# Kernel optimization log

Measured on AMD Instinct MI355X. Metric: run time of the kernel, lower is better.

The kernel has to match this reference:

```python
import jax, jax.numpy as jnp
import numpy as np

B, C, H = 16, 512, 32
HID, NB, S, P, SR = 512, 36, 26, 7, 2
SCALE = 32.0
N_LOC, N_LOC_LAB = 12, 8
N_GRP, GRP_SZ, N_GRP_LAB = 4, 6, 16
IN_DIM = P * P * C


def roi_align(feat, coords, scale, pooled, sr):
    # feat: (B,C,H,W); coords: (B,NB,4) normalized xyxy. torchvision roi_align,
    # aligned=False, fixed sampling_ratio=sr (adaptive ratio is data-dependent).
    Bs, Cc, Hh, Ww = feat.shape
    x1 = coords[..., 0] * scale
    y1 = coords[..., 1] * scale
    x2 = coords[..., 2] * scale
    y2 = coords[..., 3] * scale
    rw = jnp.maximum(x2 - x1, 1.0)
    rh = jnp.maximum(y2 - y1, 1.0)
    bw = rw / pooled
    bh = rh / pooled
    # sample offsets within roi, in bin units: (pooled*sr,)
    off = (jnp.arange(pooled)[:, None] + (jnp.arange(sr) + 0.5) / sr).reshape(-1)
    ys = y1[..., None] + off * bh[..., None]  # (B,NB,pooled*sr)
    xs = x1[..., None] + off * bw[..., None]

    def prep(t, size):
        valid = (t > -1.0) & (t < size)
        tc = jnp.clip(t, 0.0, size - 1)
        lo = jnp.floor(tc).astype(jnp.int32)
        hi = jnp.minimum(lo + 1, size - 1)
        frac = tc - lo
        return lo, hi, frac, valid

    y_lo, y_hi, ly, vy = prep(ys, Hh)
    x_lo, x_hi, lx, vx = prep(xs, Ww)
    hy, hx = 1.0 - ly, 1.0 - lx

    featl = feat.transpose(0, 2, 3, 1)  # (B,H,W,C)
    b_idx = jnp.arange(Bs)[:, None, None, None]

    def gather(yi, xi):
        # -> (B,NB,Py,Px,C)
        return featl[b_idx, yi[:, :, :, None], xi[:, :, None, :]]

    def w(a, b):
        return (a[..., :, None] * b[..., None, :])[..., None]

    val = (gather(y_lo, x_lo) * w(hy, hx) + gather(y_lo, x_hi) * w(hy, lx)
           + gather(y_hi, x_lo) * w(ly, hx) + gather(y_hi, x_hi) * w(ly, lx))
    mask = (vy[:, :, :, None] & vx[:, :, None, :])[..., None]
    val = jnp.where(mask, val, 0.0)
    val = val.reshape(Bs, -1, pooled, sr, pooled, sr, Cc).mean(axis=(3, 5))
    return val.transpose(0, 1, 4, 2, 3)  # (B,NB,C,pooled,pooled)


def setup_inputs() -> dict:
    key = jax.random.key(0)
    ks = jax.random.split(key, 10)
    lf = jax.random.normal(ks[0], (B, C, H, H), dtype=jnp.float32)
    xs = jnp.sort(jax.random.uniform(ks[1], (B, S, 2)), axis=-1)
    ys = jnp.sort(jax.random.uniform(ks[2], (B, S, 2)), axis=-1)
    coords = jnp.stack([xs[..., 0], ys[..., 0], xs[..., 1], ys[..., 1]], axis=-1)
    sc = 0.02
    return {
        'local_features': lf,
        'pred_bbox_coords': coords,
        'roi_fc_W': jax.random.normal(ks[3], (HID, IN_DIM), dtype=jnp.float32) * sc,
        'roi_fc_b': jnp.zeros((HID,), jnp.float32),
        'coords_W': jax.random.normal(ks[4], (S, 4, HID), dtype=jnp.float32) * sc,
        'coords_b': jnp.zeros((S, 4), jnp.float32),
        'pres_W': jax.random.normal(ks[5], (S, HID), dtype=jnp.float32) * sc,
        'pres_b': jnp.zeros((S,), jnp.float32),
        'loc_W': jax.random.normal(ks[6], (N_LOC, N_LOC_LAB, HID), dtype=jnp.float32) * sc,
        'loc_b': jnp.zeros((N_LOC, N_LOC_LAB), jnp.float32),
        'grp_W': jax.random.normal(ks[7], (N_GRP, N_GRP_LAB, GRP_SZ * HID), dtype=jnp.float32) * sc,
        'grp_b': jnp.zeros((N_GRP, N_GRP_LAB), jnp.float32),
        'loc_idx': jnp.arange(N_LOC, dtype=jnp.int32),
        'grp_idx': jnp.arange(N_GRP * GRP_SZ, dtype=jnp.int32).reshape(N_GRP, GRP_SZ),
    }


def reference(local_features, pred_bbox_coords, roi_fc_W, roi_fc_b, coords_W,
              coords_b, pres_W, pres_b, loc_W, loc_b, grp_W, grp_b, loc_idx, grp_idx):
    Bs = local_features.shape[0]
    # boxes S..NB default to the full image (0,0,1,1)
    full = jnp.broadcast_to(jnp.array([0.0, 0.0, 1.0, 1.0], jnp.float32), (Bs, NB, 4))
    coords_all = full.at[:, :S].set(pred_bbox_coords)
    roi = roi_align(local_features, coords_all, SCALE, P, SR)  # (B,NB,C,P,P)
    flat = roi.reshape(Bs, NB, IN_DIM)
    feats = jax.nn.relu(jnp.einsum('bnf,hf->bnh', flat, roi_fc_W) + roi_fc_b)
    sup = feats[:, :S]  # (B,S,HID)
    # per-box coord refinement heads
    deltas = jnp.einsum('bsh,soh->bso', sup, coords_W) + coords_b  # (B,S,4)
    w = pred_bbox_coords[..., 2] - pred_bbox_coords[..., 0]
    h = pred_bbox_coords[..., 3] - pred_bbox_coords[..., 1]
    wh = jnp.stack([w, h, w, h], axis=-1)
    refined = pred_bbox_coords + deltas * wh
    presence = jnp.einsum('bsh,sh->bs', sup, pres_W) + pres_b  # (B,S)
    # per-box MLC heads
    loc = jnp.einsum('blh,loh->blo', feats[:, loc_idx], loc_W) + loc_b
    # per-group MLC heads (concat box feats within group along hidden)
    gf = feats[:, grp_idx].reshape(Bs, N_GRP, GRP_SZ * HID)
    grp = jnp.einsum('bgk,gok->bgo', gf, grp_W) + grp_b
    mlc = jnp.concatenate([loc.reshape(Bs, -1), grp.reshape(Bs, -1)], axis=1)
    return refined, presence, mlc
```

## Files before the change

### kernel.cpp

```cpp
#include <hip/hip_runtime.h>

typedef unsigned short u16;
typedef __attribute__((ext_vector_type(8))) short short8;
typedef __attribute__((ext_vector_type(8))) unsigned short ushort8_t;
typedef __attribute__((ext_vector_type(4))) float f32x4;

#define BATCH   16
#define CCH     512
#define NBOX    36
#define SS      26
#define INDIM   25088
#define HIDN    512
#define M_ROWS  576
#define KSPLIT  28
#define KITERS  14

__device__ __forceinline__ u16 f2bf(float f) {
  unsigned u = __float_as_uint(f);
  u += 0x7FFF + ((u >> 16) & 1);
  return (u16)(u >> 16);
}
__device__ __forceinline__ float bf2f(u16 h) {
  return __uint_as_float(((unsigned)h) << 16);
}

typedef __attribute__((address_space(3))) void* as3_ptr;
typedef const __attribute__((address_space(1))) void* as1_cptr;
__device__ __forceinline__ void gload_lds16(const void* g, void* l) {
  __builtin_amdgcn_global_load_lds((as1_cptr)g, (as3_ptr)l, 16, 0, 0);
}

__global__ __launch_bounds__(256) void k_transpose_lf(const float* __restrict__ in,
                                                      u16* __restrict__ out) {
  __shared__ float t[32][33];
  int b = blockIdx.z, ct = blockIdx.y, pt = blockIdx.x;
  int tx = threadIdx.x, ty = threadIdx.y;
#pragma unroll
  for (int i = 0; i < 4; ++i) {
    int c = ct * 32 + ty + i * 8;
    int p = pt * 32 + tx;
    t[ty + i * 8][tx] = in[((size_t)b * CCH + c) * 1024 + p];
  }
  __syncthreads();
#pragma unroll
  for (int i = 0; i < 4; ++i) {
    int p = pt * 32 + ty + i * 8;
    int c = ct * 32 + tx;
    out[((size_t)b * 1024 + p) * CCH + c] = f2bf(t[tx][ty + i * 8]);
  }
}

__global__ __launch_bounds__(256) void k_convert_w(const float4* __restrict__ in,
                                                   ushort4* __restrict__ out) {
  int i = blockIdx.x * 256 + threadIdx.x;
  float4 v = in[i];
  ushort4 o;
  o.x = f2bf(v.x); o.y = f2bf(v.y); o.z = f2bf(v.z); o.w = f2bf(v.w);
  out[i] = o;
}

__global__ __launch_bounds__(512) void k_roi(const u16* __restrict__ lf_t,
                                             const float* __restrict__ pred,
                                             u16* __restrict__ flat) {
  __shared__ int   s_ylo[14], s_yhi[14], s_xlo[14], s_xhi[14];
  __shared__ float s_wyl[14], s_wyh[14], s_wxl[14], s_wxh[14];
  __shared__ u16   s_out[INDIM];

  int blk = blockIdx.x;
  int b = blk / NBOX, n = blk % NBOX;
  int t = threadIdx.x;

  if (t < 28) {
    bool isY = t < 14;
    int j = isY ? t : t - 14;
    float c0, c1, c2, c3;
    if (n < SS) {
      const float* p = pred + ((size_t)(b * SS + n)) * 4;
      c0 = p[0]; c1 = p[1]; c2 = p[2]; c3 = p[3];
    } else { c0 = 0.f; c1 = 0.f; c2 = 1.f; c3 = 1.f; }
    float lo1 = (isY ? c1 : c0) * 32.f;
    float hi1 = (isY ? c3 : c2) * 32.f;
    float sz = fmaxf(hi1 - lo1, 1.f);
    float bs = sz * (1.f / 7.f);
    float off = (float)(j >> 1) + 0.25f + 0.5f * (float)(j & 1);
    float pos = lo1 + off * bs;
    bool valid = (pos > -1.f) && (pos < 32.f);
    float tc = fminf(fmaxf(pos, 0.f), 31.f);
    int lo = (int)floorf(tc);
    int hi = min(lo + 1, 31);
    float fr = tc - (float)lo;
    float wl = valid ? (1.f - fr) : 0.f;
    float wh = valid ? fr : 0.f;
    if (isY) { s_ylo[j] = lo; s_yhi[j] = hi; s_wyl[j] = wl; s_wyh[j] = wh; }
    else     { s_xlo[j] = lo; s_xhi[j] = hi; s_wxl[j] = wl; s_wxh[j] = wh; }
  }
  __syncthreads();

  int cg = t & 63;
  int pg = t >> 6;
  const u16* base = lf_t + (size_t)b * 1024 * CCH + cg * 8;

  for (int p = pg; p < 49; p += 8) {
    int py = p / 7, px = p % 7;
    float a0 = 0.f, a1 = 0.f, a2 = 0.f, a3 = 0.f;
    float a4 = 0.f, a5 = 0.f, a6 = 0.f, a7 = 0.f;
#pragma unroll
    for (int sy = 0; sy < 2; ++sy) {
      int jy = 2 * py + sy;
      const u16* rlo = base + s_ylo[jy] * 32 * CCH;
      const u16* rhi = base + s_yhi[jy] * 32 * CCH;
      float wyl = s_wyl[jy], wyh = s_wyh[jy];
#pragma unroll
      for (int sx = 0; sx < 2; ++sx) {
        int jx = 2 * px + sx;
        int xl = s_xlo[jx] * CCH, xh = s_xhi[jx] * CCH;
        float wll = wyl * s_wxl[jx], wlh = wyl * s_wxh[jx];
        float whl = wyh * s_wxl[jx], whh = wyh * s_wxh[jx];
        ushort8_t vll = *(const ushort8_t*)(rlo + xl);
        ushort8_t vlh = *(const ushort8_t*)(rlo + xh);
        ushort8_t vhl = *(const ushort8_t*)(rhi + xl);
        ushort8_t vhh = *(const ushort8_t*)(rhi + xh);
        a0 += wll * bf2f(vll[0]) + wlh * bf2f(vlh[0]) + whl * bf2f(vhl[0]) + whh * bf2f(vhh[0]);
        a1 += wll * bf2f(vll[1]) + wlh * bf2f(vlh[1]) + whl * bf2f(vhl[1]) + whh * bf2f(vhh[1]);
        a2 += wll * bf2f(vll[2]) + wlh * bf2f(vlh[2]) + whl * bf2f(vhl[2]) + whh * bf2f(vhh[2]);
        a3 += wll * bf2f(vll[3]) + wlh * bf2f(vlh[3]) + whl * bf2f(vhl[3]) + whh * bf2f(vhh[3]);
        a4 += wll * bf2f(vll[4]) + wlh * bf2f(vlh[4]) + whl * bf2f(vhl[4]) + whh * bf2f(vhh[4]);
        a5 += wll * bf2f(vll[5]) + wlh * bf2f(vlh[5]) + whl * bf2f(vhl[5]) + whh * bf2f(vhh[5]);
        a6 += wll * bf2f(vll[6]) + wlh * bf2f(vlh[6]) + whl * bf2f(vhl[6]) + whh * bf2f(vhh[6]);
        a7 += wll * bf2f(vll[7]) + wlh * bf2f(vlh[7]) + whl * bf2f(vhl[7]) + whh * bf2f(vhh[7]);
      }
    }
    int c0i = cg * 8;
    s_out[(c0i + 0) * 49 + p] = f2bf(a0 * 0.25f);
    s_out[(c0i + 1) * 49 + p] = f2bf(a1 * 0.25f);
    s_out[(c0i + 2) * 49 + p] = f2bf(a2 * 0.25f);
    s_out[(c0i + 3) * 49 + p] = f2bf(a3 * 0.25f);
    s_out[(c0i + 4) * 49 + p] = f2bf(a4 * 0.25f);
    s_out[(c0i + 5) * 49 + p] = f2bf(a5 * 0.25f);
    s_out[(c0i + 6) * 49 + p] = f2bf(a6 * 0.25f);
    s_out[(c0i + 7) * 49 + p] = f2bf(a7 * 0.25f);
  }
  __syncthreads();

  uint4* dst = (uint4*)(flat + (size_t)blk * INDIM);
  const uint4* src = (const uint4*)s_out;
  for (int i = t; i < INDIM / 8; i += 512) dst[i] = src[i];
}

__global__ __launch_bounds__(256) void k_gemm(const u16* __restrict__ flat,
                                              const u16* __restrict__ Wb,
                                              float* __restrict__ partials) {
  __shared__ u16 As[128 * 64];
  __shared__ u16 Bs[128 * 64];

  int tid = threadIdx.x;
  int wave = tid >> 6, lane = tid & 63;
  int wm = wave >> 1, wn = wave & 1;
  int quad = lane >> 4, r = lane & 15;
  int xb = r & 7;

  int tileM0 = blockIdx.y * 128;
  int tileN0 = blockIdx.x * 128;
  int kbase = blockIdx.z * (KITERS * 64);

  f32x4 acc[4][4];
#pragma unroll
  for (int mi = 0; mi < 4; ++mi)
#pragma unroll
    for (int ni = 0; ni < 4; ++ni) acc[mi][ni] = (f32x4){0.f, 0.f, 0.f, 0.f};

  for (int kt = 0; kt < KITERS; ++kt) {
    int k0 = kbase + kt * 64;
#pragma unroll
    for (int t = 0; t < 4; ++t) {
      int chunk = (wave * 4 + t) * 64 + lane;
      int row = chunk >> 3;
      int pcol = chunk & 7;
      int lcol = ((pcol ^ (row & 7)) << 3);
      int grow = min(tileM0 + row, M_ROWS - 1);
      gload_lds16(flat + (size_t)grow * INDIM + k0 + lcol,
                  &As[(wave * 4 + t) * 512]);
      int nrow = tileN0 + row;
      gload_lds16(Wb + (size_t)nrow * INDIM + k0 + lcol,
                  &Bs[(wave * 4 + t) * 512]);
    }
    __syncthreads();

#pragma unroll
    for (int kk = 0; kk < 64; kk += 32) {
      int k8 = kk >> 3;
      int pc = ((k8 + quad) ^ xb) << 3;
      short8 af[4], bfr[4];
#pragma unroll
      for (int mi = 0; mi < 4; ++mi)
        af[mi] = *(const short8*)&As[(wm * 64 + mi * 16 + r) * 64 + pc];
#pragma unroll
      for (int ni = 0; ni < 4; ++ni)
        bfr[ni] = *(const short8*)&Bs[(wn * 64 + ni * 16 + r) * 64 + pc];
#pragma unroll
      for (int mi = 0; mi < 4; ++mi)
#pragma unroll
        for (int ni = 0; ni < 4; ++ni)
          acc[mi][ni] = __builtin_amdgcn_mfma_f32_16x16x32_bf16(
              af[mi], bfr[ni], acc[mi][ni], 0, 0, 0);
    }
    __syncthreads();
  }

  float* part = partials + (size_t)blockIdx.z * (M_ROWS * HIDN);
#pragma unroll
  for (int mi = 0; mi < 4; ++mi)
#pragma unroll
    for (int ni = 0; ni < 4; ++ni) {
      int row0 = tileM0 + wm * 64 + mi * 16 + quad * 4;
      int col = tileN0 + wn * 64 + ni * 16 + r;
#pragma unroll
      for (int reg = 0; reg < 4; ++reg) {
        int row = row0 + reg;
        if (row < M_ROWS) part[(size_t)row * HIDN + col] = acc[mi][ni][reg];
      }
    }
}

__global__ __launch_bounds__(256) void k_reduce(const float* __restrict__ partials,
                                                const float* __restrict__ bias,
                                                float* __restrict__ feats) {
  int gid = blockIdx.x * 256 + threadIdx.x;
  int h = gid & (HIDN - 1);
  float s = 0.f;
#pragma unroll
  for (int k = 0; k < KSPLIT; ++k) s += partials[(size_t)k * (M_ROWS * HIDN) + gid];
  s += bias[h];
  feats[gid] = fmaxf(s, 0.f);
}

__device__ __forceinline__ float wave_red(float s) {
#pragma unroll
  for (int off = 32; off > 0; off >>= 1) s += __shfl_down(s, off);
  return s;
}

__global__ __launch_bounds__(256) void k_heads(const float* __restrict__ feats,
                                               const float* __restrict__ pred,
                                               const float* __restrict__ cW,
                                               const float* __restrict__ cb,
                                               const float* __restrict__ pW,
                                               const float* __restrict__ pb,
                                               const float* __restrict__ lW,
                                               const float* __restrict__ lb,
                                               const float* __restrict__ gW,
                                               const float* __restrict__ gb,
                                               const int* __restrict__ lidx,
                                               const int* __restrict__ gidx,
                                               float* __restrict__ out) {
  int wid = blockIdx.x * 4 + (threadIdx.x >> 6);
  int lane = threadIdx.x & 63;
  float sum = 0.f;

  if (wid < 1664) {
    int b = wid / 104, rr = wid % 104, s = rr >> 2, o = rr & 3;
    const float* f = feats + (size_t)(b * NBOX + s) * HIDN;
    const float* w = cW + (size_t)(s * 4 + o) * HIDN;
#pragma unroll
    for (int i = 0; i < 8; ++i) sum += f[lane + i * 64] * w[lane + i * 64];
    sum = wave_red(sum);
    if (lane == 0) {
      const float* p = pred + (size_t)(b * SS + s) * 4;
      float wdt = p[2] - p[0], hgt = p[3] - p[1];
      float whv = (o & 1) ? hgt : wdt;
      out[wid] = p[o] + (sum + cb[s * 4 + o]) * whv;
    }
  } else if (wid < 2080) {
    int i = wid - 1664;
    int b = i / 26, s = i % 26;
    const float* f = feats + (size_t)(b * NBOX + s) * HIDN;
    const float* w = pW + (size_t)s * HIDN;
#pragma unroll
    for (int k = 0; k < 8; ++k) sum += f[lane + k * 64] * w[lane + k * 64];
    sum = wave_red(sum);
    if (lane == 0) out[1664 + i] = sum + pb[s];
  } else if (wid < 3616) {
    int i = wid - 2080;
    int b = i / 96, rr = i % 96, l = rr >> 3, o = rr & 7;
    const float* f = feats + (size_t)(b * NBOX + lidx[l]) * HIDN;
    const float* w = lW + (size_t)(l * 8 + o) * HIDN;
#pragma unroll
    for (int k = 0; k < 8; ++k) sum += f[lane + k * 64] * w[lane + k * 64];
    sum = wave_red(sum);
    if (lane == 0) out[2080 + b * 160 + rr] = sum + lb[l * 8 + o];
  } else {
    int i = wid - 3616;
    int b = i / 64, rr = i % 64, g = rr >> 4, o = rr & 15;
    const float* w = gW + (size_t)(g * 16 + o) * 3072;
#pragma unroll
    for (int jj = 0; jj < 6; ++jj) {
      const float* f = feats + (size_t)(b * NBOX + gidx[g * 6 + jj]) * HIDN;
      const float* wj = w + jj * 512;
#pragma unroll
      for (int k = 0; k < 8; ++k) sum += f[lane + k * 64] * wj[lane + k * 64];
    }
    sum = wave_red(sum);
    if (lane == 0) out[2080 + b * 160 + 96 + rr] = sum + gb[g * 16 + o];
  }
}

extern "C" void kernel_launch(void* const* d_in, const int* in_sizes, int n_in,
                              void* d_out, int out_size, void* d_ws, size_t ws_size,
                              hipStream_t stream) {
  const float* lf      = (const float*)d_in[0];
  const float* pred    = (const float*)d_in[1];
  const float* roiW    = (const float*)d_in[2];
  const float* roiB    = (const float*)d_in[3];
  const float* cW      = (const float*)d_in[4];
  const float* cb      = (const float*)d_in[5];
  const float* pW      = (const float*)d_in[6];
  const float* pb      = (const float*)d_in[7];
  const float* lW      = (const float*)d_in[8];
  const float* lb      = (const float*)d_in[9];
  const float* gW      = (const float*)d_in[10];
  const float* gb      = (const float*)d_in[11];
  const int*   lidx    = (const int*)d_in[12];
  const int*   gidx    = (const int*)d_in[13];
  float* out = (float*)d_out;

  char* ws = (char*)d_ws;
  u16*   lf_t     = (u16*)ws;
  float* partials = (float*)ws;
  u16*   Wb   = (u16*)(ws + 33030144);
  u16*   flat = (u16*)(ws + 33030144 + 25690112);
  float* feats = (float*)(ws + 33030144 + 25690112 + 28901376);

  k_transpose_lf<<<dim3(32, 16, 16), dim3(32, 8), 0, stream>>>(lf, lf_t);
  k_convert_w<<<12544, 256, 0, stream>>>((const float4*)roiW, (ushort4*)Wb);
  k_roi<<<576, 512, 0, stream>>>(lf_t, pred, flat);
  k_gemm<<<dim3(4, 5, KSPLIT), 256, 0, stream>>>(flat, Wb, partials);
  k_reduce<<<(M_ROWS * HIDN) / 256, 256, 0, stream>>>(partials, roiB, feats);
  k_heads<<<1160, 256, 0, stream>>>(feats, pred, cW, cb, pW, pb, lW, lb, gW, gb,
                                    lidx, gidx, out);
}
```

Baseline: 228.3 us.

## Halve GEMM N-tile, pack ROI bilinear math into float2, vectorize head dot products

The GEMM N tile shrinks from 128 to 64, doubling the grid in x from 560 to 1120 blocks to improve occupancy and load balance across CUs, at the cost of reloading the A tile twice as often. The ROI-align inner loop now accumulates in two-wide float vectors so the compiler can emit packed FMA instructions. The head kernels read features and weights as float4 through a shared dot512 helper instead of strided scalar loads.

Result: no change. 225.2 us (-1.4%).

```diff
diff --git a/kernel.cpp b/kernel.cpp
--- a/kernel.cpp
+++ b/kernel.cpp
@@ -4,6 +4,7 @@
 typedef __attribute__((ext_vector_type(8))) short short8;
 typedef __attribute__((ext_vector_type(8))) unsigned short ushort8_t;
 typedef __attribute__((ext_vector_type(4))) float f32x4;
+typedef __attribute__((ext_vector_type(2))) float v2f;
 
 #define BATCH   16
 #define CCH     512
@@ -22,6 +23,12 @@
 }
 __device__ __forceinline__ float bf2f(u16 h) {
   return __uint_as_float(((unsigned)h) << 16);
+}
+__device__ __forceinline__ v2f bf2x2(u16 a, u16 b) {
+  v2f r;
+  r.x = __uint_as_float(((unsigned)a) << 16);
+  r.y = __uint_as_float(((unsigned)b) << 16);
+  return r;
 }
 
 typedef __attribute__((address_space(3))) void* as3_ptr;
@@ -102,8 +109,7 @@
 
   for (int p = pg; p < 49; p += 8) {
     int py = p / 7, px = p % 7;
-    float a0 = 0.f, a1 = 0.f, a2 = 0.f, a3 = 0.f;
-    float a4 = 0.f, a5 = 0.f, a6 = 0.f, a7 = 0.f;
+    v2f a0 = {0.f, 0.f}, a1 = {0.f, 0.f}, a2 = {0.f, 0.f}, a3 = {0.f, 0.f};
 #pragma unroll
     for (int sy = 0; sy < 2; ++sy) {
       int jy = 2 * py + sy;
@@ -114,31 +120,33 @@
       for (int sx = 0; sx < 2; ++sx) {
         int jx = 2 * px + sx;
         int xl = s_xlo[jx] * CCH, xh = s_xhi[jx] * CCH;
-        float wll = wyl * s_wxl[jx], wlh = wyl * s_wxh[jx];
-        float whl = wyh * s_wxl[jx], whh = wyh * s_wxh[jx];
+        v2f wll = {wyl * s_wxl[jx], wyl * s_wxl[jx]};
+        v2f wlh = {wyl * s_wxh[jx], wyl * s_wxh[jx]};
+        v2f whl = {wyh * s_wxl[jx], wyh * s_wxl[jx]};
+        v2f whh = {wyh * s_wxh[jx], wyh * s_wxh[jx]};
         ushort8_t vll = *(const ushort8_t*)(rlo + xl);
         ushort8_t vlh = *(const ushort8_t*)(rlo + xh);
         ushort8_t vhl = *(const ushort8_t*)(rhi + xl);
         ushort8_t vhh = *(const ushort8_t*)(rhi + xh);
-        a0 += wll * bf2f(vll[0]) + wlh * bf2f(vlh[0]) + whl * bf2f(vhl[0]) + whh * bf2f(vhh[0]);
-        a1 += wll * bf2f(vll[1]) + wlh * bf2f(vlh[1]) + whl * bf2f(vhl[1]) + whh * bf2f(vhh[1]);
-        a2 += wll * bf2f(vll[2]) + wlh * bf2f(vlh[2]) + whl * bf2f(vhl[2]) + whh * bf2f(vhh[2]);
-        a3 += wll * bf2f(vll[3]) + wlh * bf2f(vlh[3]) + whl * bf2f(vhl[3]) + whh * bf2f(vhh[3]);
-        a4 += wll * bf2f(vll[4]) + wlh * bf2f(vlh[4]) + whl * bf2f(vhl[4]) + whh * bf2f(vhh[4]);
-        a5 += wll * bf2f(vll[5]) + wlh * bf2f(vlh[5]) + whl * bf2f(vhl[5]) + whh * bf2f(vhh[5]);
-        a6 += wll * bf2f(vll[6]) + wlh * bf2f(vlh[6]) + whl * bf2f(vhl[6]) + whh * bf2f(vhh[6]);
-        a7 += wll * bf2f(vll[7]) + wlh * bf2f(vlh[7]) + whl * bf2f(vhl[7]) + whh * bf2f(vhh[7]);
+        a0 += wll * bf2x2(vll[0], vll[1]) + wlh * bf2x2(vlh[0], vlh[1])
+            + whl * bf2x2(vhl[0], vhl[1]) + whh * bf2x2(vhh[0], vhh[1]);
+        a1 += wll * bf2x2(vll[2], vll[3]) + wlh * bf2x2(vlh[2], vlh[3])
+            + whl * bf2x2(vhl[2], vhl[3]) + whh * bf2x2(vhh[2], vhh[3]);
+        a2 += wll * bf2x2(vll[4], vll[5]) + wlh * bf2x2(vlh[4], vlh[5])
+            + whl * bf2x2(vhl[4], vhl[5]) + whh * bf2x2(vhh[4], vhh[5]);
+        a3 += wll * bf2x2(vll[6], vll[7]) + wlh * bf2x2(vlh[6], vlh[7])
+            + whl * bf2x2(vhl[6], vhl[7]) + whh * bf2x2(vhh[6], vhh[7]);
       }
     }
     int c0i = cg * 8;
-    s_out[(c0i + 0) * 49 + p] = f2bf(a0 * 0.25f);
-    s_out[(c0i + 1) * 49 + p] = f2bf(a1 * 0.25f);
-    s_out[(c0i + 2) * 49 + p] = f2bf(a2 * 0.25f);
-    s_out[(c0i + 3) * 49 + p] = f2bf(a3 * 0.25f);
-    s_out[(c0i + 4) * 49 + p] = f2bf(a4 * 0.25f);
-    s_out[(c0i + 5) * 49 + p] = f2bf(a5 * 0.25f);
-    s_out[(c0i + 6) * 49 + p] = f2bf(a6 * 0.25f);
-    s_out[(c0i + 7) * 49 + p] = f2bf(a7 * 0.25f);
+    s_out[(c0i + 0) * 49 + p] = f2bf(a0.x * 0.25f);
+    s_out[(c0i + 1) * 49 + p] = f2bf(a0.y * 0.25f);
+    s_out[(c0i + 2) * 49 + p] = f2bf(a1.x * 0.25f);
+    s_out[(c0i + 3) * 49 + p] = f2bf(a1.y * 0.25f);
+    s_out[(c0i + 4) * 49 + p] = f2bf(a2.x * 0.25f);
+    s_out[(c0i + 5) * 49 + p] = f2bf(a2.y * 0.25f);
+    s_out[(c0i + 6) * 49 + p] = f2bf(a3.x * 0.25f);
+    s_out[(c0i + 7) * 49 + p] = f2bf(a3.y * 0.25f);
   }
   __syncthreads();
 
@@ -151,7 +159,7 @@
                                               const u16* __restrict__ Wb,
                                               float* __restrict__ partials) {
   __shared__ u16 As[128 * 64];
-  __shared__ u16 Bs[128 * 64];
+  __shared__ u16 Bs[64 * 64];
 
   int tid = threadIdx.x;
   int wave = tid >> 6, lane = tid & 63;
@@ -160,14 +168,14 @@
   int xb = r & 7;
 
   int tileM0 = blockIdx.y * 128;
-  int tileN0 = blockIdx.x * 128;
+  int tileN0 = blockIdx.x * 64;
   int kbase = blockIdx.z * (KITERS * 64);
 
-  f32x4 acc[4][4];
+  f32x4 acc[4][2];
 #pragma unroll
   for (int mi = 0; mi < 4; ++mi)
 #pragma unroll
-    for (int ni = 0; ni < 4; ++ni) acc[mi][ni] = (f32x4){0.f, 0.f, 0.f, 0.f};
+    for (int ni = 0; ni < 2; ++ni) acc[mi][ni] = (f32x4){0.f, 0.f, 0.f, 0.f};
 
   for (int kt = 0; kt < KITERS; ++kt) {
     int k0 = kbase + kt * 64;
@@ -180,9 +188,16 @@
       int grow = min(tileM0 + row, M_ROWS - 1);
       gload_lds16(flat + (size_t)grow * INDIM + k0 + lcol,
                   &As[(wave * 4 + t) * 512]);
+    }
+#pragma unroll
+    for (int t = 0; t < 2; ++t) {
+      int chunk = (wave * 2 + t) * 64 + lane;
+      int row = chunk >> 3;
+      int pcol = chunk & 7;
+      int lcol = ((pcol ^ (row & 7)) << 3);
       int nrow = tileN0 + row;
       gload_lds16(Wb + (size_t)nrow * INDIM + k0 + lcol,
-                  &Bs[(wave * 4 + t) * 512]);
+                  &Bs[(wave * 2 + t) * 512]);
     }
     __syncthreads();
 
@@ -190,17 +205,17 @@
     for (int kk = 0; kk < 64; kk += 32) {
       int k8 = kk >> 3;
       int pc = ((k8 + quad) ^ xb) << 3;
-      short8 af[4], bfr[4];
+      short8 af[4], bfr[2];
 #pragma unroll
       for (int mi = 0; mi < 4; ++mi)
         af[mi] = *(const short8*)&As[(wm * 64 + mi * 16 + r) * 64 + pc];
 #pragma unroll
-      for (int ni = 0; ni < 4; ++ni)
-        bfr[ni] = *(const short8*)&Bs[(wn * 64 + ni * 16 + r) * 64 + pc];
+      for (int ni = 0; ni < 2; ++ni)
+        bfr[ni] = *(const short8*)&Bs[(wn * 32 + ni * 16 + r) * 64 + pc];
 #pragma unroll
       for (int mi = 0; mi < 4; ++mi)
 #pragma unroll
-        for (int ni = 0; ni < 4; ++ni)
+        for (int ni = 0; ni < 2; ++ni)
           acc[mi][ni] = __builtin_amdgcn_mfma_f32_16x16x32_bf16(
               af[mi], bfr[ni], acc[mi][ni], 0, 0, 0);
     }
@@ -211,9 +226,9 @@
 #pragma unroll
   for (int mi = 0; mi < 4; ++mi)
 #pragma unroll
-    for (int ni = 0; ni < 4; ++ni) {
+    for (int ni = 0; ni < 2; ++ni) {
       int row0 = tileM0 + wm * 64 + mi * 16 + quad * 4;
-      int col = tileN0 + wn * 64 + ni * 16 + r;
+      int col = tileN0 + wn * 32 + ni * 16 + r;
 #pragma unroll
       for (int reg = 0; reg < 4; ++reg) {
         int row = row0 + reg;
@@ -238,6 +253,16 @@
 #pragma unroll
   for (int off = 32; off > 0; off >>= 1) s += __shfl_down(s, off);
   return s;
+}
+
+__device__ __forceinline__ float dot512(const float* __restrict__ f,
+                                        const float* __restrict__ w, int lane) {
+  const float4* f4 = (const float4*)f;
+  const float4* w4 = (const float4*)w;
+  float4 x0 = f4[lane], y0 = w4[lane];
+  float4 x1 = f4[lane + 64], y1 = w4[lane + 64];
+  return x0.x * y0.x + x0.y * y0.y + x0.z * y0.z + x0.w * y0.w +
+         x1.x * y1.x + x1.y * y1.y + x1.z * y1.z + x1.w * y1.w;
 }
 
 __global__ __launch_bounds__(256) void k_heads(const float* __restrict__ feats,
@@ -259,10 +284,8 @@
 
   if (wid < 1664) {
     int b = wid / 104, rr = wid % 104, s = rr >> 2, o = rr & 3;
-    const float* f = feats + (size_t)(b * NBOX + s) * HIDN;
-    const float* w = cW + (size_t)(s * 4 + o) * HIDN;
-#pragma unroll
-    for (int i = 0; i < 8; ++i) sum += f[lane + i * 64] * w[lane + i * 64];
+    sum = dot512(feats + (size_t)(b * NBOX + s) * HIDN,
+                 cW + (size_t)(s * 4 + o) * HIDN, lane);
     sum = wave_red(sum);
     if (lane == 0) {
       const float* p = pred + (size_t)(b * SS + s) * 4;
@@ -273,19 +296,15 @@
   } else if (wid < 2080) {
     int i = wid - 1664;
     int b = i / 26, s = i % 26;
-    const float* f = feats + (size_t)(b * NBOX + s) * HIDN;
-    const float* w = pW + (size_t)s * HIDN;
-#pragma unroll
-    for (int k = 0; k < 8; ++k) sum += f[lane + k * 64] * w[lane + k * 64];
+    sum = dot512(feats + (size_t)(b * NBOX + s) * HIDN,
+                 pW + (size_t)s * HIDN, lane);
     sum = wave_red(sum);
     if (lane == 0) out[1664 + i] = sum + pb[s];
   } else if (wid < 3616) {
     int i = wid - 2080;
     int b = i / 96, rr = i % 96, l = rr >> 3, o = rr & 7;
-    const float* f = feats + (size_t)(b * NBOX + lidx[l]) * HIDN;
-    const float* w = lW + (size_t)(l * 8 + o) * HIDN;
-#pragma unroll
-    for (int k = 0; k < 8; ++k) sum += f[lane + k * 64] * w[lane + k * 64];
+    sum = dot512(feats + (size_t)(b * NBOX + lidx[l]) * HIDN,
+                 lW + (size_t)(l * 8 + o) * HIDN, lane);
     sum = wave_red(sum);
     if (lane == 0) out[2080 + b * 160 + rr] = sum + lb[l * 8 + o];
   } else {
@@ -294,10 +313,8 @@
     const float* w = gW + (size_t)(g * 16 + o) * 3072;
 #pragma unroll
     for (int jj = 0; jj < 6; ++jj) {
-      const float* f = feats + (size_t)(b * NBOX + gidx[g * 6 + jj]) * HIDN;
-      const float* wj = w + jj * 512;
-#pragma unroll
-      for (int k = 0; k < 8; ++k) sum += f[lane + k * 64] * wj[lane + k * 64];
+      sum += dot512(feats + (size_t)(b * NBOX + gidx[g * 6 + jj]) * HIDN,
+                    w + jj * 512, lane);
     }
     sum = wave_red(sum);
     if (lane == 0) out[2080 + b * 160 + 96 + rr] = sum + gb[g * 16 + o];
@@ -333,7 +350,7 @@
   k_transpose_lf<<<dim3(32, 16, 16), dim3(32, 8), 0, stream>>>(lf, lf_t);
   k_convert_w<<<12544, 256, 0, stream>>>((const float4*)roiW, (ushort4*)Wb);
   k_roi<<<576, 512, 0, stream>>>(lf_t, pred, flat);
-  k_gemm<<<dim3(4, 5, KSPLIT), 256, 0, stream>>>(flat, Wb, partials);
+  k_gemm<<<dim3(8, 5, KSPLIT), 256, 0, stream>>>(flat, Wb, partials);
   k_reduce<<<(M_ROWS * HIDN) / 256, 256, 0, stream>>>(partials, roiB, feats);
   k_heads<<<1160, 256, 0, stream>>>(feats, pred, cW, cb, pW, pb, lW, lb, gW, gb,
                                     lidx, gidx, out);
```
